# Performance work log

Hardware: AMD Instinct MI355X
Metric: run time of the kernel (lower is better)

The kernel has to match this reference:

```python
import jax, jax.numpy as jnp
import numpy as np

B, T, D, H, NL, DFF = 8, 255, 1024, 16, 8, 4096
DH = D // H
STD = 0.02


def setup_inputs() -> dict:
    key = jax.random.key(0)
    ks = jax.random.split(key, 16)
    n = lambda k, shape, s=STD: jax.random.normal(k, shape, dtype=jnp.float32) * s
    return {
        "x": n(ks[0], (B, T, D), 1.0),
        "mask": jnp.ones((B, T), dtype=jnp.int64),
        "is_train": 0,
        "sum_emb": n(ks[1], (1, D)),
        "modality_emb": n(ks[2], (T + 1, D)),
        "ln1_w": jnp.ones((NL, D), jnp.float32),
        "ln1_b": jnp.zeros((NL, D), jnp.float32),
        "w_qkv": n(ks[3], (NL, D, 3 * D)),
        "b_qkv": jnp.zeros((NL, 3 * D), jnp.float32),
        "w_proj": n(ks[4], (NL, D, D), STD / np.sqrt(2 * NL)),
        "b_proj": jnp.zeros((NL, D), jnp.float32),
        "ln2_w": jnp.ones((NL, D), jnp.float32),
        "ln2_b": jnp.zeros((NL, D), jnp.float32),
        "w_fc": n(ks[5], (NL, D, DFF)),
        "b_fc": jnp.zeros((NL, DFF), jnp.float32),
        "w_out": n(ks[6], (NL, DFF, D), STD / np.sqrt(2 * NL)),
        "b_out": jnp.zeros((NL, D), jnp.float32),
        "norm_w": jnp.ones((D,), jnp.float32),
        "norm_b": jnp.zeros((D,), jnp.float32),
    }


def _ln(x, w, b, eps=1e-5):
    m = x.mean(-1, keepdims=True)
    v = ((x - m) ** 2).mean(-1, keepdims=True)
    return (x - m) / jnp.sqrt(v + eps) * w + b


def reference(x, mask, is_train, sum_emb, modality_emb, ln1_w, ln1_b, w_qkv, b_qkv,
              w_proj, b_proj, ln2_w, ln2_b, w_fc, b_fc, w_out, b_out, norm_w, norm_b):
    b, t, d = x.shape
    L = t + 1
    # prepend summary token + its mask bit, add modality (position) embedding
    summ = jnp.broadcast_to(sum_emb[None, :, :], (b, 1, d))
    h = jnp.concatenate([summ, x], axis=1) + modality_emb[None, :, :]  # [B,L,D]
    full_mask = jnp.concatenate([jnp.ones((b, 1), mask.dtype), mask], axis=1)  # [B,L]
    key_bias = jnp.where(full_mask[:, None, None, :] == 1, 0.0, -1e9)  # [B,1,1,L]
    # is_train==0: random input-drop loop is a no-op in eval mode

    def block(h, p):
        l1w, l1b, wq, bq, wp, bp, l2w, l2b, wf, bf, wo, bo = p
        a = _ln(h, l1w, l1b)
        qkv = a @ wq + bq
        q, k, v = jnp.split(qkv, 3, axis=-1)
        q = q.reshape(b, L, H, DH).transpose(0, 2, 1, 3)
        k = k.reshape(b, L, H, DH).transpose(0, 2, 1, 3)
        v = v.reshape(b, L, H, DH).transpose(0, 2, 1, 3)
        scores = jnp.einsum("bhqd,bhkd->bhqk", q, k) / np.sqrt(DH) + key_bias
        att = jax.nn.softmax(scores, axis=-1)  # [B,H,L,L]
        y = jnp.einsum("bhqk,bhkd->bhqd", att, v).transpose(0, 2, 1, 3).reshape(b, L, d)
        h = h + y @ wp + bp
        m = _ln(h, l2w, l2b)
        h = h + jax.nn.gelu(m @ wf + bf) @ wo + bo
        return h, att

    params = (ln1_w, ln1_b, w_qkv, b_qkv, w_proj, b_proj, ln2_w, ln2_b, w_fc, b_fc, w_out, b_out)
    h, all_att = jax.lax.scan(block, h, params)
    h = _ln(h, norm_w, norm_b)
    return h[:, 0], all_att
```

## Files before the change

### kernel.cpp

```cpp
#include <hip/hip_runtime.h>


using u16 = unsigned short;
typedef __attribute__((ext_vector_type(8))) __bf16 bf16x8;
typedef __attribute__((ext_vector_type(4))) float f32x4;
typedef __attribute__((ext_vector_type(8))) unsigned short ushort8;

__device__ __forceinline__ u16 f2b(float f) {
  unsigned u = __builtin_bit_cast(unsigned, f);
  return (u16)((u + 0x7FFFu + ((u >> 16) & 1u)) >> 16);
}

__device__ __forceinline__ bf16x8 ldfrag(const u16* p) {
  return *reinterpret_cast<const bf16x8*>(p);
}

__device__ __forceinline__ f32x4 mfma16(bf16x8 a, bf16x8 b, f32x4 c) {
  return __builtin_amdgcn_mfma_f32_16x16x32_bf16(a, b, c, 0, 0, 0);
}

__device__ __forceinline__ void gload16(const void* g, void* l) {
  __builtin_amdgcn_global_load_lds(
      (const __attribute__((address_space(1))) unsigned int*)g,
      (__attribute__((address_space(3))) unsigned int*)l, 16, 0, 0);
}

__global__ __launch_bounds__(256) void embed_k(
    const float* __restrict__ x, const float* __restrict__ sum_emb,
    const float* __restrict__ mod_emb, float* __restrict__ h) {
  int idx = blockIdx.x * 256 + threadIdx.x;
  int d = idx & 1023;
  int l = (idx >> 10) & 255;
  int b = idx >> 18;
  float v = (l == 0) ? sum_emb[d] : x[(size_t)(b * 255 + l - 1) * 1024 + d];
  h[idx] = v + mod_emb[l * 1024 + d];
}

__global__ __launch_bounds__(256) void transpose_w(
    const float* __restrict__ in, u16* __restrict__ out, int R, int C) {
  __shared__ float tile[32][33];
  const int t = threadIdx.x;
  const int r0 = blockIdx.y * 32, c0 = blockIdx.x * 32;
  const int tr = t >> 5, tc = t & 31;
#pragma unroll
  for (int i = 0; i < 4; ++i)
    tile[tr + i * 8][tc] = in[(size_t)(r0 + tr + i * 8) * C + c0 + tc];
  __syncthreads();
#pragma unroll
  for (int i = 0; i < 4; ++i) {
    int cc = tr + i * 8, rr = tc;
    out[(size_t)(c0 + cc) * R + r0 + rr] = f2b(tile[rr][cc]);
  }
}

__global__ __launch_bounds__(256) void ln_bf16(
    const float* __restrict__ x, const float* __restrict__ w,
    const float* __restrict__ bb, u16* __restrict__ out) {
  const int r = blockIdx.x, t = threadIdx.x;
  const float* xr = x + (size_t)r * 1024;
  float v[4], s1 = 0.f, s2 = 0.f;
#pragma unroll
  for (int i = 0; i < 4; ++i) {
    v[i] = xr[t + i * 256];
    s1 += v[i];
    s2 += v[i] * v[i];
  }
#pragma unroll
  for (int o = 32; o > 0; o >>= 1) {
    s1 += __shfl_down(s1, o);
    s2 += __shfl_down(s2, o);
  }
  __shared__ float red[8];
  const int wv = t >> 6, l = t & 63;
  if (l == 0) { red[wv] = s1; red[4 + wv] = s2; }
  __syncthreads();
  s1 = red[0] + red[1] + red[2] + red[3];
  s2 = red[4] + red[5] + red[6] + red[7];
  float mean = s1 * (1.0f / 1024.0f);
  float var = s2 * (1.0f / 1024.0f) - mean * mean;
  float rstd = rsqrtf(var + 1e-5f);
#pragma unroll
  for (int i = 0; i < 4; ++i) {
    int c = t + i * 256;
    out[(size_t)r * 1024 + c] = f2b((v[i] - mean) * rstd * w[c] + bb[c]);
  }
}

__global__ __launch_bounds__(256) void final_ln(
    const float* __restrict__ h, const float* __restrict__ w,
    const float* __restrict__ bb, float* __restrict__ out) {
  const int r = blockIdx.x, t = threadIdx.x;
  const float* xr = h + (size_t)r * 262144;
  float v[4], s1 = 0.f, s2 = 0.f;
#pragma unroll
  for (int i = 0; i < 4; ++i) {
    v[i] = xr[t + i * 256];
    s1 += v[i];
    s2 += v[i] * v[i];
  }
#pragma unroll
  for (int o = 32; o > 0; o >>= 1) {
    s1 += __shfl_down(s1, o);
    s2 += __shfl_down(s2, o);
  }
  __shared__ float red[8];
  const int wv = t >> 6, l = t & 63;
  if (l == 0) { red[wv] = s1; red[4 + wv] = s2; }
  __syncthreads();
  s1 = red[0] + red[1] + red[2] + red[3];
  s2 = red[4] + red[5] + red[6] + red[7];
  float mean = s1 * (1.0f / 1024.0f);
  float var = s2 * (1.0f / 1024.0f) - mean * mean;
  float rstd = rsqrtf(var + 1e-5f);
#pragma unroll
  for (int i = 0; i < 4; ++i) {
    int c = t + i * 256;
    out[r * 1024 + c] = (v[i] - mean) * rstd * w[c] + bb[c];
  }
}

template <int EPI>
__global__ __launch_bounds__(256) void gemm_bt(
    const u16* __restrict__ A, const u16* __restrict__ BT,
    const float* __restrict__ bias, float* __restrict__ Hres,
    u16* __restrict__ Obf, int M, int N, int K) {
  __shared__ u16 As[128 * 32];
  __shared__ u16 Bs[128 * 32];
  const int t = threadIdx.x;
  const int m0 = blockIdx.y * 128, n0 = blockIdx.x * 128;
  const int l = t & 63, w = t >> 6;
  const int wr = (w >> 1) * 64, wc = (w & 1) * 64;
  const int lr = l & 15, lh = l >> 4;

  const int srow = t >> 2;
  const int skc = (t & 3) * 8;
  const u16* Ag = A + (size_t)(m0 + srow) * K + skc;
  const u16* Bg = BT + (size_t)(n0 + srow) * K + skc;

  f32x4 acc[4][4] = {};
  const int nk = K / 32;
  for (int kt = 0; kt < nk; ++kt) {
    __syncthreads();
    gload16(Ag, As + t * 8);
    gload16(Ag + (size_t)64 * K, As + 2048 + t * 8);
    gload16(Bg, Bs + t * 8);
    gload16(Bg + (size_t)64 * K, Bs + 2048 + t * 8);
    Ag += 32;
    Bg += 32;
    __syncthreads();
    bf16x8 af[4], bfr[4];
#pragma unroll
    for (int m = 0; m < 4; ++m) af[m] = ldfrag(As + (wr + m * 16 + lr) * 32 + lh * 8);
#pragma unroll
    for (int n = 0; n < 4; ++n) bfr[n] = ldfrag(Bs + (wc + n * 16 + lr) * 32 + lh * 8);
#pragma unroll
    for (int m = 0; m < 4; ++m)
#pragma unroll
      for (int n = 0; n < 4; ++n) acc[m][n] = mfma16(af[m], bfr[n], acc[m][n]);
  }
#pragma unroll
  for (int m = 0; m < 4; ++m) {
#pragma unroll
    for (int n = 0; n < 4; ++n) {
      const int col = n0 + wc + n * 16 + lr;
      const float bc = bias[col];
#pragma unroll
      for (int j = 0; j < 4; ++j) {
        const int row = m0 + wr + m * 16 + lh * 4 + j;
        float v = acc[m][n][j] + bc;
        if (EPI == 0) {
          Obf[(size_t)row * N + col] = f2b(v);
        } else if (EPI == 1) {
          size_t idx = (size_t)row * N + col;
          Hres[idx] = Hres[idx] + v;
        } else {
          float g = 0.5f * v *
                    (1.0f + tanhf(0.7978845608028654f * (v + 0.044715f * v * v * v)));
          Obf[(size_t)row * N + col] = f2b(g);
        }
      }
    }
  }
}

__global__ __launch_bounds__(256) void attn_qk(
    const u16* __restrict__ qkv, const int* __restrict__ mask,
    float* __restrict__ att_out, u16* __restrict__ att_bf) {
  __shared__ u16 Qs[32 * 64];
  __shared__ u16 Ks[256 * 64];
  __shared__ float Sf[32 * 256];
  __shared__ float mbias[256];
  __shared__ float rmax[32], rsum[32];
  const int t = threadIdx.x;
  const int blk = blockIdx.x;
  const int qt = blk & 7, hh = (blk >> 3) & 15, b = blk >> 7;
  const int q0 = qt * 32;

  mbias[t] = (t == 0) ? 0.0f : ((mask[b * 255 + t - 1] == 1) ? 0.0f : -1e9f);

  {
    int row = t >> 3, c = t & 7;
    int gcol = (c ^ (row & 7)) * 8;
    gload16(qkv + (size_t)(b * 256 + q0 + row) * 3072 + hh * 64 + gcol, Qs + t * 8);
  }
#pragma unroll
  for (int s = 0; s < 8; ++s) {
    int row = s * 32 + (t >> 3), c = t & 7;
    int gcol = (c ^ (row & 7)) * 8;
    gload16(qkv + (size_t)(b * 256 + row) * 3072 + 1024 + hh * 64 + gcol,
            Ks + s * 2048 + t * 8);
  }
  __syncthreads();

  const int l = t & 63, w = t >> 6;
  const int lr = l & 15, lh = l >> 4;
  const int c0 = w * 64;
  f32x4 acc[2][4] = {};
#pragma unroll
  for (int ks = 0; ks < 2; ++ks) {
    bf16x8 af[2], bfr[4];
#pragma unroll
    for (int m = 0; m < 2; ++m) {
      int row = m * 16 + lr;
      int chunk = (ks * 4 + lh) ^ (row & 7);
      af[m] = ldfrag(Qs + row * 64 + chunk * 8);
    }
#pragma unroll
    for (int n = 0; n < 4; ++n) {
      int row = c0 + n * 16 + lr;
      int chunk = (ks * 4 + lh) ^ (row & 7);
      bfr[n] = ldfrag(Ks + row * 64 + chunk * 8);
    }
#pragma unroll
    for (int m = 0; m < 2; ++m)
#pragma unroll
      for (int n = 0; n < 4; ++n) acc[m][n] = mfma16(af[m], bfr[n], acc[m][n]);
  }
#pragma unroll
  for (int m = 0; m < 2; ++m)
#pragma unroll
    for (int n = 0; n < 4; ++n) {
      const int col = c0 + n * 16 + lr;
      const float mb = mbias[col];
#pragma unroll
      for (int j = 0; j < 4; ++j) {
        int row = m * 16 + lh * 4 + j;
        Sf[row * 256 + col] = acc[m][n][j] * 0.125f + mb;
      }
    }
  __syncthreads();

  {
    const int row = t >> 3, tg = t & 7;
    float mx = -1e30f;
#pragma unroll 8
    for (int k = 0; k < 32; ++k) {
      int c = tg * 32 + ((k + row * 4 + tg) & 31);
      mx = fmaxf(mx, Sf[row * 256 + c]);
    }
    mx = fmaxf(mx, __shfl_xor(mx, 1));
    mx = fmaxf(mx, __shfl_xor(mx, 2));
    mx = fmaxf(mx, __shfl_xor(mx, 4));
    float sm = 0.f;
#pragma unroll 8
    for (int k = 0; k < 32; ++k) {
      int c = tg * 32 + ((k + row * 4 + tg) & 31);
      sm += expf(Sf[row * 256 + c] - mx);
    }
    sm += __shfl_xor(sm, 1);
    sm += __shfl_xor(sm, 2);
    sm += __shfl_xor(sm, 4);
    if (tg == 0) {
      rmax[row] = mx;
      rsum[row] = 1.0f / sm;
    }
  }
  __syncthreads();

  const size_t obase = ((size_t)b * 16 + hh) * 65536 + (size_t)q0 * 256;
#pragma unroll 4
  for (int i = 0; i < 32; ++i) {
    float p = expf(Sf[i * 256 + t] - rmax[i]) * rsum[i];
    att_out[obase + (size_t)i * 256 + t] = p;
    att_bf[obase + (size_t)i * 256 + t] = f2b(p);
  }
}

#define VS 264
__global__ __launch_bounds__(256) void attn_pv(
    const u16* __restrict__ qkv, const u16* __restrict__ att_bf,
    u16* __restrict__ y) {
  __shared__ u16 Vt[64 * VS];
  const int t = threadIdx.x;
  const int b = blockIdx.x >> 4, hh = blockIdx.x & 15;
  const int l = t & 63, w = t >> 6;
  {
    const int j = w * 64 + l;
    const u16* vsrc = qkv + (size_t)(b * 256 + j) * 3072 + 2048 + hh * 64;
#pragma unroll
    for (int dd = 0; dd < 8; ++dd) {
      ushort8 v = *reinterpret_cast<const ushort8*>(vsrc + dd * 8);
#pragma unroll
      for (int e = 0; e < 8; ++e) Vt[(dd * 8 + e) * VS + j] = v[e];
    }
  }
  __syncthreads();
  const int lr = l & 15, lh = l >> 4;
  const int r0 = w * 64;
  const u16* Pg = att_bf + ((size_t)(b * 16 + hh)) * 65536;
  f32x4 acc[4][4] = {};
#pragma unroll
  for (int ks = 0; ks < 8; ++ks) {
    bf16x8 af[4], bfr[4];
#pragma unroll
    for (int m = 0; m < 4; ++m)
      af[m] = ldfrag(Pg + (size_t)(r0 + m * 16 + lr) * 256 + ks * 32 + lh * 8);
#pragma unroll
    for (int n = 0; n < 4; ++n)
      bfr[n] = ldfrag(Vt + (n * 16 + lr) * VS + ks * 32 + lh * 8);
#pragma unroll
    for (int m = 0; m < 4; ++m)
#pragma unroll
      for (int n = 0; n < 4; ++n) acc[m][n] = mfma16(af[m], bfr[n], acc[m][n]);
  }
#pragma unroll
  for (int m = 0; m < 4; ++m)
#pragma unroll
    for (int n = 0; n < 4; ++n)
#pragma unroll
      for (int j = 0; j < 4; ++j) {
        int row = r0 + m * 16 + lh * 4 + j;
        int col = n * 16 + lr;
        y[(size_t)(b * 256 + row) * 1024 + hh * 64 + col] = f2b(acc[m][n][j]);
      }
}

extern "C" void kernel_launch(void* const* d_in, const int* in_sizes, int n_in,
                              void* d_out, int out_size, void* d_ws, size_t ws_size,
                              hipStream_t stream) {
  (void)in_sizes; (void)n_in; (void)out_size; (void)ws_size;
  const float* x      = (const float*)d_in[0];
  const int* mask     = (const int*)d_in[1];
  const float* sum_emb = (const float*)d_in[3];
  const float* mod_emb = (const float*)d_in[4];
  const float* ln1_w  = (const float*)d_in[5];
  const float* ln1_b  = (const float*)d_in[6];
  const float* w_qkv  = (const float*)d_in[7];
  const float* b_qkv  = (const float*)d_in[8];
  const float* w_proj = (const float*)d_in[9];
  const float* b_proj = (const float*)d_in[10];
  const float* ln2_w  = (const float*)d_in[11];
  const float* ln2_b  = (const float*)d_in[12];
  const float* w_fc   = (const float*)d_in[13];
  const float* b_fc   = (const float*)d_in[14];
  const float* w_out  = (const float*)d_in[15];
  const float* b_out  = (const float*)d_in[16];
  const float* norm_w = (const float*)d_in[17];
  const float* norm_b = (const float*)d_in[18];

  char* ws = (char*)d_ws;
  float* h    = (float*)(ws + 0);
  u16* wqkvT  = (u16*)(ws + 8388608);
  u16* wprojT = (u16*)(ws + 14680064);
  u16* wfcT   = (u16*)(ws + 16777216);
  u16* woutT  = (u16*)(ws + 25165824);
  u16* a_bf   = (u16*)(ws + 33554432);
  u16* qkv_bf = (u16*)(ws + 37748736);
  u16* att_bf = (u16*)(ws + 50331648);
  u16* y_bf   = (u16*)(ws + 67108864);
  u16* g_bf   = (u16*)(ws + 71303168);
  float* att_f = (float*)d_out + 8192;

  embed_k<<<8192, 256, 0, stream>>>(x, sum_emb, mod_emb, h);

  for (int L = 0; L < 8; ++L) {
    const float* wqkv_l = w_qkv + (size_t)L * 1024 * 3072;
    const float* wproj_l = w_proj + (size_t)L * 1024 * 1024;
    const float* wfc_l = w_fc + (size_t)L * 1024 * 4096;
    const float* wout_l = w_out + (size_t)L * 4096 * 1024;

    transpose_w<<<dim3(96, 32), 256, 0, stream>>>(wqkv_l, wqkvT, 1024, 3072);
    transpose_w<<<dim3(32, 32), 256, 0, stream>>>(wproj_l, wprojT, 1024, 1024);
    transpose_w<<<dim3(128, 32), 256, 0, stream>>>(wfc_l, wfcT, 1024, 4096);
    transpose_w<<<dim3(32, 128), 256, 0, stream>>>(wout_l, woutT, 4096, 1024);

    ln_bf16<<<2048, 256, 0, stream>>>(h, ln1_w + L * 1024, ln1_b + L * 1024, a_bf);
    gemm_bt<0><<<dim3(24, 16), 256, 0, stream>>>(a_bf, wqkvT, b_qkv + L * 3072,
                                                 nullptr, qkv_bf, 2048, 3072, 1024);
    attn_qk<<<1024, 256, 0, stream>>>(qkv_bf, mask, att_f + (size_t)L * 8388608,
                                      att_bf);
    attn_pv<<<128, 256, 0, stream>>>(qkv_bf, att_bf, y_bf);
    gemm_bt<1><<<dim3(8, 16), 256, 0, stream>>>(y_bf, wprojT, b_proj + L * 1024, h,
                                                nullptr, 2048, 1024, 1024);
    ln_bf16<<<2048, 256, 0, stream>>>(h, ln2_w + L * 1024, ln2_b + L * 1024, a_bf);
    gemm_bt<2><<<dim3(32, 16), 256, 0, stream>>>(a_bf, wfcT, b_fc + L * 4096,
                                                 nullptr, g_bf, 2048, 4096, 1024);
    gemm_bt<1><<<dim3(8, 16), 256, 0, stream>>>(g_bf, woutT, b_out + L * 1024, h,
                                                nullptr, 2048, 1024, 4096);
  }

  final_ln<<<8, 256, 0, stream>>>(h, norm_w, norm_b, (float*)d_out);
}
```

Before: 2.512 ms.

## Fuse attention QK and PV, split-K residual GEMMs, batch weight transposes

Merges the attention score/softmax kernel with the P·V kernel so the bf16 probability matrix is no longer written to and re-read from global memory. V is staged transposed in shared memory and probabilities are recomputed from the scores buffer, which gets a swizzled index. The two residual GEMMs with small grids gain split-K via blockIdx.z and atomicAdd into h, raising occupancy at the cost of nondeterministic float summation. When the workspace is large enough, weight transposes for all layers run once up front in batched launches rather than per layer.

```diff
diff --git a/kernel.cpp b/kernel.cpp
--- a/kernel.cpp
+++ b/kernel.cpp
@@ -39,6 +39,8 @@
 __global__ __launch_bounds__(256) void transpose_w(
     const float* __restrict__ in, u16* __restrict__ out, int R, int C) {
   __shared__ float tile[32][33];
+  in += (size_t)blockIdx.z * R * C;
+  out += (size_t)blockIdx.z * R * C;
   const int t = threadIdx.x;
   const int r0 = blockIdx.y * 32, c0 = blockIdx.x * 32;
   const int tr = t >> 5, tc = t & 31;
@@ -119,7 +121,7 @@
   }
 }
 
-template <int EPI>
+template <int EPI, int SPLIT>
 __global__ __launch_bounds__(256) void gemm_bt(
     const u16* __restrict__ A, const u16* __restrict__ BT,
     const float* __restrict__ bias, float* __restrict__ Hres,
@@ -128,6 +130,10 @@
   __shared__ u16 Bs[128 * 32];
   const int t = threadIdx.x;
   const int m0 = blockIdx.y * 128, n0 = blockIdx.x * 128;
+  const int Kl = K / SPLIT;
+  const int kz = (SPLIT > 1) ? blockIdx.z : 0;
+  A += (size_t)kz * Kl;
+  BT += (size_t)kz * Kl;
   const int l = t & 63, w = t >> 6;
   const int wr = (w >> 1) * 64, wc = (w & 1) * 64;
   const int lr = l & 15, lh = l >> 4;
@@ -138,7 +144,7 @@
   const u16* Bg = BT + (size_t)(n0 + srow) * K + skc;
 
   f32x4 acc[4][4] = {};
-  const int nk = K / 32;
+  const int nk = Kl / 32;
   for (int kt = 0; kt < nk; ++kt) {
     __syncthreads();
     gload16(Ag, As + t * 8);
@@ -163,7 +169,7 @@
 #pragma unroll
     for (int n = 0; n < 4; ++n) {
       const int col = n0 + wc + n * 16 + lr;
-      const float bc = bias[col];
+      const float bc = (SPLIT == 1 || kz == 0) ? bias[col] : 0.0f;
 #pragma unroll
       for (int j = 0; j < 4; ++j) {
         const int row = m0 + wr + m * 16 + lh * 4 + j;
@@ -172,7 +178,8 @@
           Obf[(size_t)row * N + col] = f2b(v);
         } else if (EPI == 1) {
           size_t idx = (size_t)row * N + col;
-          Hres[idx] = Hres[idx] + v;
+          if (SPLIT == 1) Hres[idx] = Hres[idx] + v;
+          else atomicAdd(Hres + idx, v);
         } else {
           float g = 0.5f * v *
                     (1.0f + tanhf(0.7978845608028654f * (v + 0.044715f * v * v * v)));
@@ -183,11 +190,16 @@
   }
 }
 
-__global__ __launch_bounds__(256) void attn_qk(
+#define VS 264
+__device__ __forceinline__ int sfi(int row, int col) {
+  return row * 256 + ((col & 7) | (((col >> 3) ^ (row & 7)) << 3));
+}
+
+__global__ __launch_bounds__(256) void attn_fused(
     const u16* __restrict__ qkv, const int* __restrict__ mask,
-    float* __restrict__ att_out, u16* __restrict__ att_bf) {
+    float* __restrict__ att_out, u16* __restrict__ y) {
   __shared__ u16 Qs[32 * 64];
-  __shared__ u16 Ks[256 * 64];
+  __shared__ u16 KV[64 * VS];
   __shared__ float Sf[32 * 256];
   __shared__ float mbias[256];
   __shared__ float rmax[32], rsum[32];
@@ -208,65 +220,71 @@
     int row = s * 32 + (t >> 3), c = t & 7;
     int gcol = (c ^ (row & 7)) * 8;
     gload16(qkv + (size_t)(b * 256 + row) * 3072 + 1024 + hh * 64 + gcol,
-            Ks + s * 2048 + t * 8);
+            KV + s * 2048 + t * 8);
   }
   __syncthreads();
 
   const int l = t & 63, w = t >> 6;
   const int lr = l & 15, lh = l >> 4;
-  const int c0 = w * 64;
-  f32x4 acc[2][4] = {};
-#pragma unroll
-  for (int ks = 0; ks < 2; ++ks) {
-    bf16x8 af[2], bfr[4];
-#pragma unroll
-    for (int m = 0; m < 2; ++m) {
-      int row = m * 16 + lr;
-      int chunk = (ks * 4 + lh) ^ (row & 7);
-      af[m] = ldfrag(Qs + row * 64 + chunk * 8);
-    }
-#pragma unroll
-    for (int n = 0; n < 4; ++n) {
-      int row = c0 + n * 16 + lr;
-      int chunk = (ks * 4 + lh) ^ (row & 7);
-      bfr[n] = ldfrag(Ks + row * 64 + chunk * 8);
+  {
+    const int c0 = w * 64;
+    f32x4 acc[2][4] = {};
+#pragma unroll
+    for (int ks = 0; ks < 2; ++ks) {
+      bf16x8 af[2], bfr[4];
+#pragma unroll
+      for (int m = 0; m < 2; ++m) {
+        int row = m * 16 + lr;
+        int chunk = (ks * 4 + lh) ^ (row & 7);
+        af[m] = ldfrag(Qs + row * 64 + chunk * 8);
+      }
+#pragma unroll
+      for (int n = 0; n < 4; ++n) {
+        int row = c0 + n * 16 + lr;
+        int chunk = (ks * 4 + lh) ^ (row & 7);
+        bfr[n] = ldfrag(KV + row * 64 + chunk * 8);
+      }
+#pragma unroll
+      for (int m = 0; m < 2; ++m)
+#pragma unroll
+        for (int n = 0; n < 4; ++n) acc[m][n] = mfma16(af[m], bfr[n], acc[m][n]);
     }
 #pragma unroll
     for (int m = 0; m < 2; ++m)
 #pragma unroll
-      for (int n = 0; n < 4; ++n) acc[m][n] = mfma16(af[m], bfr[n], acc[m][n]);
-  }
-#pragma unroll
-  for (int m = 0; m < 2; ++m)
-#pragma unroll
-    for (int n = 0; n < 4; ++n) {
-      const int col = c0 + n * 16 + lr;
-      const float mb = mbias[col];
-#pragma unroll
-      for (int j = 0; j < 4; ++j) {
-        int row = m * 16 + lh * 4 + j;
-        Sf[row * 256 + col] = acc[m][n][j] * 0.125f + mb;
-      }
-    }
-  __syncthreads();
+      for (int n = 0; n < 4; ++n) {
+        const int col = c0 + n * 16 + lr;
+        const float mb = mbias[col];
+#pragma unroll
+        for (int j = 0; j < 4; ++j) {
+          int row = m * 16 + lh * 4 + j;
+          Sf[sfi(row, col)] = acc[m][n][j] * 0.125f + mb;
+        }
+      }
+  }
+  __syncthreads();
+
+  ushort8 vreg[4][2];
+#pragma unroll
+  for (int s = 0; s < 4; ++s) {
+    const int j = s * 64 + (t >> 2);
+    const u16* vsrc =
+        qkv + (size_t)(b * 256 + j) * 3072 + 2048 + hh * 64 + (t & 3) * 16;
+    vreg[s][0] = *reinterpret_cast<const ushort8*>(vsrc);
+    vreg[s][1] = *reinterpret_cast<const ushort8*>(vsrc + 8);
+  }
 
   {
     const int row = t >> 3, tg = t & 7;
     float mx = -1e30f;
 #pragma unroll 8
-    for (int k = 0; k < 32; ++k) {
-      int c = tg * 32 + ((k + row * 4 + tg) & 31);
-      mx = fmaxf(mx, Sf[row * 256 + c]);
-    }
+    for (int k = 0; k < 32; ++k) mx = fmaxf(mx, Sf[sfi(row, tg * 32 + k)]);
     mx = fmaxf(mx, __shfl_xor(mx, 1));
     mx = fmaxf(mx, __shfl_xor(mx, 2));
     mx = fmaxf(mx, __shfl_xor(mx, 4));
     float sm = 0.f;
 #pragma unroll 8
-    for (int k = 0; k < 32; ++k) {
-      int c = tg * 32 + ((k + row * 4 + tg) & 31);
-      sm += expf(Sf[row * 256 + c] - mx);
-    }
+    for (int k = 0; k < 32; ++k) sm += __expf(Sf[sfi(row, tg * 32 + k)] - mx);
     sm += __shfl_xor(sm, 1);
     sm += __shfl_xor(sm, 2);
     sm += __shfl_xor(sm, 4);
@@ -275,70 +293,66 @@
       rsum[row] = 1.0f / sm;
     }
   }
+
+#pragma unroll
+  for (int s = 0; s < 4; ++s) {
+    const int j = s * 64 + (t >> 2);
+    const int d0 = (t & 3) * 16;
+#pragma unroll
+    for (int e = 0; e < 8; ++e) {
+      KV[(d0 + e) * VS + j] = vreg[s][0][e];
+      KV[(d0 + 8 + e) * VS + j] = vreg[s][1][e];
+    }
+  }
   __syncthreads();
 
   const size_t obase = ((size_t)b * 16 + hh) * 65536 + (size_t)q0 * 256;
 #pragma unroll 4
   for (int i = 0; i < 32; ++i) {
-    float p = expf(Sf[i * 256 + t] - rmax[i]) * rsum[i];
+    float p = __expf(Sf[sfi(i, t)] - rmax[i]) * rsum[i];
     att_out[obase + (size_t)i * 256 + t] = p;
-    att_bf[obase + (size_t)i * 256 + t] = f2b(p);
-  }
-}
-
-#define VS 264
-__global__ __launch_bounds__(256) void attn_pv(
-    const u16* __restrict__ qkv, const u16* __restrict__ att_bf,
-    u16* __restrict__ y) {
-  __shared__ u16 Vt[64 * VS];
-  const int t = threadIdx.x;
-  const int b = blockIdx.x >> 4, hh = blockIdx.x & 15;
-  const int l = t & 63, w = t >> 6;
+  }
+
   {
-    const int j = w * 64 + l;
-    const u16* vsrc = qkv + (size_t)(b * 256 + j) * 3072 + 2048 + hh * 64;
-#pragma unroll
-    for (int dd = 0; dd < 8; ++dd) {
-      ushort8 v = *reinterpret_cast<const ushort8*>(vsrc + dd * 8);
-#pragma unroll
-      for (int e = 0; e < 8; ++e) Vt[(dd * 8 + e) * VS + j] = v[e];
-    }
-  }
-  __syncthreads();
-  const int lr = l & 15, lh = l >> 4;
-  const int r0 = w * 64;
-  const u16* Pg = att_bf + ((size_t)(b * 16 + hh)) * 65536;
-  f32x4 acc[4][4] = {};
-#pragma unroll
-  for (int ks = 0; ks < 8; ++ks) {
-    bf16x8 af[4], bfr[4];
-#pragma unroll
-    for (int m = 0; m < 4; ++m)
-      af[m] = ldfrag(Pg + (size_t)(r0 + m * 16 + lr) * 256 + ks * 32 + lh * 8);
-#pragma unroll
-    for (int n = 0; n < 4; ++n)
-      bfr[n] = ldfrag(Vt + (n * 16 + lr) * VS + ks * 32 + lh * 8);
-#pragma unroll
-    for (int m = 0; m < 4; ++m)
-#pragma unroll
-      for (int n = 0; n < 4; ++n) acc[m][n] = mfma16(af[m], bfr[n], acc[m][n]);
-  }
-#pragma unroll
-  for (int m = 0; m < 4; ++m)
-#pragma unroll
-    for (int n = 0; n < 4; ++n)
+    const int mrow = (w & 1) * 16;
+    const int n0c = (w >> 1) * 32;
+    const int rr = mrow + lr;
+    const float mxl = rmax[rr], rsl = rsum[rr];
+    f32x4 acc2[2] = {};
+#pragma unroll
+    for (int ks = 0; ks < 8; ++ks) {
+      const int kbase = ks * 32 + lh * 8;
+      const int ch = (kbase >> 3) ^ (rr & 7);
+      const float* sp = &Sf[rr * 256 + ch * 8];
+      f32x4 s0 = *reinterpret_cast<const f32x4*>(sp);
+      f32x4 s1 = *reinterpret_cast<const f32x4*>(sp + 4);
+      ushort8 pu;
+#pragma unroll
+      for (int e = 0; e < 4; ++e) pu[e] = f2b(__expf(s0[e] - mxl) * rsl);
+#pragma unroll
+      for (int e = 0; e < 4; ++e) pu[4 + e] = f2b(__expf(s1[e] - mxl) * rsl);
+      bf16x8 af = __builtin_bit_cast(bf16x8, pu);
+#pragma unroll
+      for (int n = 0; n < 2; ++n) {
+        bf16x8 bfr = ldfrag(KV + (n0c + n * 16 + lr) * VS + kbase);
+        acc2[n] = mfma16(af, bfr, acc2[n]);
+      }
+    }
+#pragma unroll
+    for (int n = 0; n < 2; ++n)
 #pragma unroll
       for (int j = 0; j < 4; ++j) {
-        int row = r0 + m * 16 + lh * 4 + j;
-        int col = n * 16 + lr;
-        y[(size_t)(b * 256 + row) * 1024 + hh * 64 + col] = f2b(acc[m][n][j]);
-      }
+        int row = mrow + lh * 4 + j;
+        int col = n0c + n * 16 + lr;
+        y[(size_t)(b * 256 + q0 + row) * 1024 + hh * 64 + col] = f2b(acc2[n][j]);
+      }
+  }
 }
 
 extern "C" void kernel_launch(void* const* d_in, const int* in_sizes, int n_in,
                               void* d_out, int out_size, void* d_ws, size_t ws_size,
                               hipStream_t stream) {
-  (void)in_sizes; (void)n_in; (void)out_size; (void)ws_size;
+  (void)in_sizes; (void)n_in; (void)out_size;
   const float* x      = (const float*)d_in[0];
   const int* mask     = (const int*)d_in[1];
   const float* sum_emb = (const float*)d_in[3];
@@ -360,43 +374,54 @@
 
   char* ws = (char*)d_ws;
   float* h    = (float*)(ws + 0);
-  u16* wqkvT  = (u16*)(ws + 8388608);
-  u16* wprojT = (u16*)(ws + 14680064);
-  u16* wfcT   = (u16*)(ws + 16777216);
-  u16* woutT  = (u16*)(ws + 25165824);
-  u16* a_bf   = (u16*)(ws + 33554432);
-  u16* qkv_bf = (u16*)(ws + 37748736);
-  u16* att_bf = (u16*)(ws + 50331648);
-  u16* y_bf   = (u16*)(ws + 67108864);
-  u16* g_bf   = (u16*)(ws + 71303168);
+  u16* a_bf   = (u16*)(ws + 8388608);
+  u16* qkv_bf = (u16*)(ws + 12582912);
+  u16* y_bf   = (u16*)(ws + 25165824);
+  u16* g_bf   = (u16*)(ws + 29360128);
+  u16* wqkvT  = (u16*)(ws + 46137344);
+  u16* wprojT = (u16*)(ws + 96468992);
+  u16* wfcT   = (u16*)(ws + 113246208);
+  u16* woutT  = (u16*)(ws + 180355072);
   float* att_f = (float*)d_out + 8192;
 
+  const bool big = ws_size >= 248000000ull;
+  const size_t stq = big ? (size_t)3072 * 1024 : 0;
+  const size_t stp = big ? (size_t)1024 * 1024 : 0;
+  const size_t stf = big ? (size_t)4096 * 1024 : 0;
+  const size_t sto = big ? (size_t)4096 * 1024 : 0;
+
   embed_k<<<8192, 256, 0, stream>>>(x, sum_emb, mod_emb, h);
 
+  if (big) {
+    transpose_w<<<dim3(96, 32, 8), 256, 0, stream>>>(w_qkv, wqkvT, 1024, 3072);
+    transpose_w<<<dim3(32, 32, 8), 256, 0, stream>>>(w_proj, wprojT, 1024, 1024);
+    transpose_w<<<dim3(128, 32, 8), 256, 0, stream>>>(w_fc, wfcT, 1024, 4096);
+    transpose_w<<<dim3(32, 128, 8), 256, 0, stream>>>(w_out, woutT, 4096, 1024);
+  }
+
   for (int L = 0; L < 8; ++L) {
-    const float* wqkv_l = w_qkv + (size_t)L * 1024 * 3072;
-    const float* wproj_l = w_proj + (size_t)L * 1024 * 1024;
-    const float* wfc_l = w_fc + (size_t)L * 1024 * 4096;
-    const float* wout_l = w_out + (size_t)L * 4096 * 1024;
-
-    transpose_w<<<dim3(96, 32), 256, 0, stream>>>(wqkv_l, wqkvT, 1024, 3072);
-    transpose_w<<<dim3(32, 32), 256, 0, stream>>>(wproj_l, wprojT, 1024, 1024);
-    transpose_w<<<dim3(128, 32), 256, 0, stream>>>(wfc_l, wfcT, 1024, 4096);
-    transpose_w<<<dim3(32, 128), 256, 0, stream>>>(wout_l, woutT, 4096, 1024);
-
+    if (!big) {
+      transpose_w<<<dim3(96, 32, 1), 256, 0, stream>>>(
+          w_qkv + (size_t)L * 1024 * 3072, wqkvT, 1024, 3072);
+      transpose_w<<<dim3(32, 32, 1), 256, 0, stream>>>(
+          w_proj + (size_t)L * 1024 * 1024, wprojT, 1024, 1024);
+      transpose_w<<<dim3(128, 32, 1), 256, 0, stream>>>(
+          w_fc + (size_t)L * 1024 * 4096, wfcT, 1024, 4096);
+      transpose_w<<<dim3(32, 128, 1), 256, 0, stream>>>(
+          w_out + (size_t)L * 4096 * 1024, woutT, 4096, 1024);
+    }
     ln_bf16<<<2048, 256, 0, stream>>>(h, ln1_w + L * 1024, ln1_b + L * 1024, a_bf);
-    gemm_bt<0><<<dim3(24, 16), 256, 0, stream>>>(a_bf, wqkvT, b_qkv + L * 3072,
-                                                 nullptr, qkv_bf, 2048, 3072, 1024);
-    attn_qk<<<1024, 256, 0, stream>>>(qkv_bf, mask, att_f + (size_t)L * 8388608,
-                                      att_bf);
-    attn_pv<<<128, 256, 0, stream>>>(qkv_bf, att_bf, y_bf);
-    gemm_bt<1><<<dim3(8, 16), 256, 0, stream>>>(y_bf, wprojT, b_proj + L * 1024, h,
-                                                nullptr, 2048, 1024, 1024);
+    gemm_bt<0, 1><<<dim3(24, 16, 1), 256, 0, stream>>>(
+        a_bf, wqkvT + L * stq, b_qkv + L * 3072, nullptr, qkv_bf, 2048, 3072, 1024);
+    attn_fused<<<1024, 256, 0, stream>>>(qkv_bf, mask,
+                                         att_f + (size_t)L * 8388608, y_bf);
+    gemm_bt<1, 2><<<dim3(8, 16, 2), 256, 0, stream>>>(
+        y_bf, wprojT + L * stp, b_proj + L * 1024, h, nullptr, 2048, 1024, 1024);
     ln_bf16<<<2048, 256, 0, stream>>>(h, ln2_w + L * 1024, ln2_b + L * 1024, a_bf);
-    gemm_bt<2><<<dim3(32, 16), 256, 0, stream>>>(a_bf, wfcT, b_fc + L * 4096,
-                                                 nullptr, g_bf, 2048, 4096, 1024);
-    gemm_bt<1><<<dim3(8, 16), 256, 0, stream>>>(g_bf, woutT, b_out + L * 1024, h,
-                                                nullptr, 2048, 1024, 4096);
+    gemm_bt<2, 1><<<dim3(32, 16, 1), 256, 0, stream>>>(
+        a_bf, wfcT + L * stf, b_fc + L * 4096, nullptr, g_bf, 2048, 4096, 1024);
+    gemm_bt<1, 4><<<dim3(8, 16, 4), 256, 0, stream>>>(
+        g_bf, woutT + L * sto, b_out + L * 1024, h, nullptr, 2048, 1024, 4096);
   }
 
   final_ln<<<8, 256, 0, stream>>>(h, norm_w, norm_b, (float*)d_out);
```

Result: faster. 2.110 ms (-16.0%).
